# Optimization experiments

Measured on AMD Instinct MI355X. Metric: run time of the kernel, lower is better.

Reference implementation:

```python
import jax, jax.numpy as jnp
import numpy as np

N = 131072          # flattened ray-sample points
C = 32              # output_coordinate_dim per plane
BASE = 128          # base grid resolution
SCALES = [1, 2, 4]  # multiscale_res multipliers
HID = 256           # ResBlock / CondMLP hidden width
OUT = 16            # decoder output dim (geo features)
COMBS = [(0, 1), (0, 2), (1, 2)]  # itertools.combinations(range(3), 2)


def setup_inputs() -> dict:
    key = jax.random.key(0)
    ks = iter(jax.random.split(key, 64))
    inp = {}
    inp['pts'] = jax.random.uniform(next(ks), (N, 3), dtype=jnp.float32)
    inp['aabb'] = jnp.asarray([[0.0, 0.0, 0.0], [1.0, 1.0, 1.0]], dtype=jnp.float32)
    # 9 plane grids: 3 scales x 3 coordinate combinations, uniform in [0.1, 0.5)
    for s, mult in enumerate(SCALES):
        r = BASE * mult
        for ci in range(3):
            inp[f'plane_{s}_{ci}'] = jax.random.uniform(
                next(ks), (C, r, r), dtype=jnp.float32, minval=0.1, maxval=0.5)
    feat_dim = C * len(SCALES)  # concat across scales -> 96
    def lin(k, fin, fout):
        bound = 1.0 / np.sqrt(fin)
        kw, kb = jax.random.split(k)
        w = jax.random.uniform(kw, (fin, fout), dtype=jnp.float32, minval=-bound, maxval=bound)
        b = jax.random.uniform(kb, (fout,), dtype=jnp.float32, minval=-bound, maxval=bound)
        return w, b
    inp['l0_w'], inp['l0_b'] = lin(next(ks), feat_dim, HID)
    # 3 ResBlocks x 3 linears (lz, l1, l2), all 256x256 -> stacked
    rw, rb = [], []
    for _ in range(9):
        w, b = lin(next(ks), HID, HID)
        rw.append(w); rb.append(b)
    inp['res_w'] = jnp.stack(rw).reshape(3, 3, HID, HID)
    inp['res_b'] = jnp.stack(rb).reshape(3, 3, HID)
    inp['l1_w'], inp['l1_b'] = lin(next(ks), HID, OUT)
    return inp


def _bilinear(plane, xy):
    # plane: [C, H, W]; xy: [N, 2] in [-1, 1]; x -> W axis, y -> H axis
    # (F.grid_sample, align_corners=True; border clamp == zeros pad since pts in-bounds)
    Cc, H, W = plane.shape
    x = (xy[:, 0] + 1.0) * 0.5 * (W - 1)
    y = (xy[:, 1] + 1.0) * 0.5 * (H - 1)
    x0 = jnp.clip(jnp.floor(x), 0, W - 2).astype(jnp.int32)
    y0 = jnp.clip(jnp.floor(y), 0, H - 2).astype(jnp.int32)
    x1, y1 = x0 + 1, y0 + 1
    wx = (x - x0)[None, :]
    wy = (y - y0)[None, :]
    v = (plane[:, y0, x0] * (1 - wx) * (1 - wy)
         + plane[:, y0, x1] * wx * (1 - wy)
         + plane[:, y1, x0] * (1 - wx) * wy
         + plane[:, y1, x1] * wx * wy)          # [C, N]
    return v.T                                   # [N, C]


def _interp_ms(xn, planes):
    # planes: list of 3 scales, each a list of 3 [C,H,W] grids
    feats = []
    for scale_planes in planes:
        interp = 1.0
        for plane, (c0, c1) in zip(scale_planes, COMBS):
            xy = jnp.stack([xn[:, c0], xn[:, c1]], axis=-1)
            interp = interp * _bilinear(plane, xy)  # hadamard across planes
        feats.append(interp)
    return jnp.concatenate(feats, axis=-1)          # [N, C*num_scales]


def _cond_mlp(f, l0_w, l0_b, res_w, res_b, l1_w, l1_b):
    x = f @ l0_w + l0_b
    for i in range(3):
        z = jax.nn.relu(x @ res_w[i, 0] + res_b[i, 0])
        res = x + z
        x = jax.nn.relu(res @ res_w[i, 1] + res_b[i, 1])
        x = jax.nn.relu(x @ res_w[i, 2] + res_b[i, 2]) + res
    return jax.nn.sigmoid(x @ l1_w + l1_b)


def reference(pts, aabb,
              plane_0_0, plane_0_1, plane_0_2,
              plane_1_0, plane_1_1, plane_1_2,
              plane_2_0, plane_2_1, plane_2_2,
              l0_w, l0_b, res_w, res_b, l1_w, l1_b):
    xn = (pts - aabb[0]) * (2.0 / (aabb[1] - aabb[0])) - 1.0  # normalize_aabb
    planes = [[plane_0_0, plane_0_1, plane_0_2],
              [plane_1_0, plane_1_1, plane_1_2],
              [plane_2_0, plane_2_1, plane_2_2]]
    feats = _interp_ms(xn, planes)                            # [N, 96]
    return _cond_mlp(feats, l0_w, l0_b, res_w, res_b, l1_w, l1_b)  # [N, 16]
```

## Files before the change

### kernel.cpp

```cpp
#include <hip/hip_runtime.h>

typedef unsigned short u16;
typedef unsigned int u32;
typedef __attribute__((ext_vector_type(2))) unsigned int u32x2;
typedef __attribute__((ext_vector_type(8))) short short8;
typedef __attribute__((ext_vector_type(8))) _Float16 half8;
typedef __attribute__((ext_vector_type(2))) __fp16 fp16x2;
typedef __attribute__((ext_vector_type(4))) float floatx4;

__device__ __forceinline__ u16 f2h(float f){ _Float16 h = (_Float16)f; return __builtin_bit_cast(u16, h); }
__device__ __forceinline__ u32 pkrtz(float a, float b){
  fp16x2 h = __builtin_amdgcn_cvt_pkrtz(a, b);
  return __builtin_bit_cast(u32, h);
}
__device__ __forceinline__ u32 pkmax0(u32 a){
  u32 d, z = 0;
  asm("v_pk_max_f16 %0, %1, %2" : "=v"(d) : "v"(a), "v"(z));
  return d;
}
__device__ __forceinline__ u32 pkadd(u32 a, u32 b){
  u32 d;
  asm("v_pk_add_f16 %0, %1, %2" : "=v"(d) : "v"(a), "v"(b));
  return d;
}

__global__ void ptrans_kernel(const float* __restrict__ src, u16* __restrict__ dst, int HW){
  __shared__ float tile[32][257];
  const int t = threadIdx.x;
  const size_t hw0 = (size_t)blockIdx.x * 256;
  #pragma unroll
  for (int c = 0; c < 32; c++) tile[c][t] = src[(size_t)c*HW + hw0 + t];
  __syncthreads();
  u32* d32 = (u32*)(dst + hw0*32);
  #pragma unroll
  for (int i = 0; i < 16; i++){
    int idx = i*512 + t*2;
    int j = idx >> 5, cc = idx & 31;
    u32 lo = f2h(tile[cc][j]);
    u32 hi = f2h(tile[cc+1][j]);
    d32[i*256 + t] = lo | (hi << 16);
  }
}

__global__ void wconv_kernel(const float* __restrict__ src, u16* __restrict__ dst,
                             int fin, int fout, int total){
  int t = blockIdx.x*256 + threadIdx.x;
  if (t >= total) return;
  int per = fin * fout;
  int m = t / per, r = t - m*per;
  int KS = fin >> 5;
  int e = r & 7;
  int lane = (r >> 3) & 63;
  int fs = r >> 9;
  int ks = fs % KS, ft = fs / KS;
  int of = ft*16 + (lane & 15);
  int k  = ks*32 + (lane >> 4)*8 + e;
  dst[t] = f2h(src[(size_t)m*per + (size_t)k*fout + of]);
}

struct PlanePtrs { const void* p[9]; };

__global__ void interp4_kernel(const float* __restrict__ pts, const float* __restrict__ aabb,
                               PlanePtrs pp, u16* __restrict__ feats, int N)
{
  int g = blockIdx.x*256 + threadIdx.x;
  int n = g >> 2, v = g & 3;
  if (n >= N) return;
  float xn[3];
  #pragma unroll
  for (int d=0; d<3; d++){
    float lo = aabb[d], hi = aabb[3+d];
    xn[d] = (pts[(size_t)n*3 + d] - lo) * (2.0f/(hi - lo)) - 1.0f;
  }
  const int c0s[3] = {0,0,1};
  const int c1s[3] = {1,2,2};
  #pragma unroll
  for (int s=0; s<3; s++){
    const int R = 128 << s;
    float prod[8];
    #pragma unroll
    for (int p=0; p<3; p++){
      float fx = (xn[c0s[p]] + 1.0f) * 0.5f * (float)(R-1);
      float fy = (xn[c1s[p]] + 1.0f) * 0.5f * (float)(R-1);
      float fx0 = fminf(fmaxf(floorf(fx), 0.0f), (float)(R-2));
      float fy0 = fminf(fmaxf(floorf(fy), 0.0f), (float)(R-2));
      int x0 = (int)fx0, y0 = (int)fy0;
      float wx = fx - fx0, wy = fy - fy0;
      float w00 = (1.0f-wx)*(1.0f-wy), w01 = wx*(1.0f-wy);
      float w10 = (1.0f-wx)*wy,        w11 = wx*wy;
      const u16* base = (const u16*)pp.p[s*3 + p];
      const u16* b00 = base + ((size_t)y0*R + x0)*32 + v*8;
      const u16* b10 = b00 + (size_t)R*32;
      half8 h00 = *(const half8*)b00;
      half8 h01 = *(const half8*)(b00 + 32);
      half8 h10 = *(const half8*)b10;
      half8 h11 = *(const half8*)(b10 + 32);
      #pragma unroll
      for (int e=0; e<8; e++){
        float val = (float)h00[e]*w00 + (float)h01[e]*w01 + (float)h10[e]*w10 + (float)h11[e]*w11;
        prod[e] = (p == 0) ? val : prod[e]*val;
      }
    }
    short8 pk8;
    #pragma unroll
    for (int e=0; e<8; e++) pk8[e] = (short)f2h(prod[e]);
    *(short8*)(feats + (size_t)n*96 + s*32 + v*8) = pk8;
  }
}

__global__ void interp_fb_kernel(const float* __restrict__ pts, const float* __restrict__ aabb,
                                 PlanePtrs pp, u16* __restrict__ feats, int N)
{
  int n = blockIdx.x*256 + threadIdx.x;
  if (n >= N) return;
  float xn[3];
  #pragma unroll
  for (int d=0; d<3; d++){
    float lo = aabb[d], hi = aabb[3+d];
    xn[d] = (pts[(size_t)n*3 + d] - lo) * (2.0f/(hi - lo)) - 1.0f;
  }
  const int c0s[3] = {0,0,1};
  const int c1s[3] = {1,2,2};
  #pragma unroll
  for (int s=0; s<3; s++){
    const int R = 128 << s;
    float prod[32];
    #pragma unroll
    for (int p=0; p<3; p++){
      float fx = (xn[c0s[p]] + 1.0f) * 0.5f * (float)(R-1);
      float fy = (xn[c1s[p]] + 1.0f) * 0.5f * (float)(R-1);
      float fx0 = fminf(fmaxf(floorf(fx), 0.0f), (float)(R-2));
      float fy0 = fminf(fmaxf(floorf(fy), 0.0f), (float)(R-2));
      int x0 = (int)fx0, y0 = (int)fy0;
      float wx = fx - fx0, wy = fy - fy0;
      float w00 = (1.0f-wx)*(1.0f-wy), w01 = wx*(1.0f-wy);
      float w10 = (1.0f-wx)*wy,        w11 = wx*wy;
      const size_t HW = (size_t)R*R;
      const float* b00f = (const float*)pp.p[s*3+p] + (size_t)y0*R + x0;
      #pragma unroll 4
      for (int c=0; c<32; c++){
        const float* q = b00f + (size_t)c*HW;
        float val = q[0]*w00 + q[1]*w01 + q[R]*w10 + q[R+1]*w11;
        prod[c] = (p == 0) ? val : prod[c]*val;
      }
    }
    #pragma unroll
    for (int vv=0; vv<4; vv++){
      short8 pk8;
      #pragma unroll
      for (int e=0; e<8; e++) pk8[e] = (short)f2h(prod[vv*8+e]);
      *(short8*)(feats + (size_t)n*96 + s*32 + vv*8) = pk8;
    }
  }
}

template<int KSTEPS>
__device__ __forceinline__ void mm_tile(const u16* X, const u16* __restrict__ WTs,
                                        int ftbase, int lane, const floatx4 binit[4],
                                        floatx4 acc[4][4])
{
  const int lr = lane & 15, lg = lane >> 4;
  #pragma unroll
  for (int rf=0; rf<4; rf++)
    #pragma unroll
    for (int cf=0; cf<4; cf++)
      acc[rf][cf] = binit[rf];
  #pragma unroll 1
  for (int ks=0; ks<KSTEPS; ks++){
    half8 w[4];
    #pragma unroll
    for (int rf=0; rf<4; rf++)
      w[rf] = *(const half8*)(WTs + ((size_t)((ftbase+rf)*KSTEPS + ks)*64 + lane)*8);
    half8 x[4];
    #pragma unroll
    for (int cf=0; cf<4; cf++){
      int pt = cf*16 + lr;
      int byt = (pt*512 + (ks*32 + lg*8)*2) ^ ((pt & 7) << 4);
      x[cf] = *(const half8*)((const char*)X + byt);
    }
    __builtin_amdgcn_s_setprio(1);
    #pragma unroll
    for (int rf=0; rf<4; rf++)
      #pragma unroll
      for (int cf=0; cf<4; cf++)
        acc[rf][cf] = __builtin_amdgcn_mfma_f32_16x16x32_f16(w[rf], x[cf], acc[rf][cf], 0, 0, 0);
    __builtin_amdgcn_s_setprio(0);
  }
}

__device__ __forceinline__ void load_binit(const float* b, int wb, int rf16, int lg, floatx4* bi){
  #pragma unroll
  for (int rf=0; rf<4; rf++){
    float4 v = *(const float4*)(b + wb + rf*16 + lg*4);
    bi[rf] = (floatx4){v.x, v.y, v.z, v.w};
  }
  (void)rf16;
}

__global__ __launch_bounds__(256, 2) void mlp_kernel(
    const u16* __restrict__ feats,
    const u16* __restrict__ l0T, const u16* __restrict__ resT, const u16* __restrict__ l1T,
    const float* __restrict__ l0_b, const float* __restrict__ res_b, const float* __restrict__ l1_b,
    float* __restrict__ out)
{
  __shared__ u16 Xb[2][64*256];
  const int tid = threadIdx.x;
  const int wave = tid >> 6, lane = tid & 63;
  const int lr = lane & 15, lg = lane >> 4;
  const int n0 = blockIdx.x * 64;
  const int ftbase = wave * 4;
  const int wb = wave * 64;

  #pragma unroll
  for (int i=0; i<3; i++){
    int id = tid + i*256;
    int row = id / 12, sub = id - row*12;
    short8 v = *(const short8*)(feats + (size_t)(n0+row)*96 + sub*8);
    int byt = (row*512 + sub*16) ^ ((row & 7) << 4);
    *(short8*)((char*)Xb[0] + byt) = v;
  }
  __syncthreads();

  floatx4 acc[4][4];
  floatx4 binit[4];
  u32 pk[4][4][2];
  int cur = 0;

  load_binit(l0_b, wb, 0, lg, binit);
  mm_tile<3>(Xb[0], l0T, ftbase, lane, binit, acc);
  {
    char* Xw = (char*)Xb[1];
    #pragma unroll
    for (int rf=0; rf<4; rf++){
      int fby = (wb + rf*16 + lg*4)*2;
      #pragma unroll
      for (int cf=0; cf<4; cf++){
        int pt = cf*16 + lr;
        u32 p0 = pkrtz(acc[rf][cf][0], acc[rf][cf][1]);
        u32 p1 = pkrtz(acc[rf][cf][2], acc[rf][cf][3]);
        pk[rf][cf][0] = p0; pk[rf][cf][1] = p1;
        int byt = (pt*512 + fby) ^ ((pt & 7) << 4);
        *(u32x2*)(Xw + byt) = (u32x2){p0, p1};
      }
    }
  }
  __syncthreads();
  cur = 1;

  for (int rb=0; rb<3; rb++){
    const u16* W0 = resT + (size_t)(rb*3+0)*65536;
    const u16* W1 = resT + (size_t)(rb*3+1)*65536;
    const u16* W2 = resT + (size_t)(rb*3+2)*65536;
    const float* b0 = res_b + (rb*3+0)*256;
    const float* b1 = res_b + (rb*3+1)*256;
    const float* b2 = res_b + (rb*3+2)*256;

    load_binit(b0, wb, 0, lg, binit);
    mm_tile<8>(Xb[cur], W0, ftbase, lane, binit, acc);
    {
      char* Xw = (char*)Xb[cur^1];
      #pragma unroll
      for (int rf=0; rf<4; rf++){
        int fby = (wb + rf*16 + lg*4)*2;
        #pragma unroll
        for (int cf=0; cf<4; cf++){
          int pt = cf*16 + lr;
          u32 p0 = pkadd(pk[rf][cf][0], pkmax0(pkrtz(acc[rf][cf][0], acc[rf][cf][1])));
          u32 p1 = pkadd(pk[rf][cf][1], pkmax0(pkrtz(acc[rf][cf][2], acc[rf][cf][3])));
          pk[rf][cf][0] = p0; pk[rf][cf][1] = p1;
          int byt = (pt*512 + fby) ^ ((pt & 7) << 4);
          *(u32x2*)(Xw + byt) = (u32x2){p0, p1};
        }
      }
    }
    __syncthreads();
    cur ^= 1;

    load_binit(b1, wb, 0, lg, binit);
    mm_tile<8>(Xb[cur], W1, ftbase, lane, binit, acc);
    {
      char* Xw = (char*)Xb[cur^1];
      #pragma unroll
      for (int rf=0; rf<4; rf++){
        int fby = (wb + rf*16 + lg*4)*2;
        #pragma unroll
        for (int cf=0; cf<4; cf++){
          int pt = cf*16 + lr;
          u32 p0 = pkmax0(pkrtz(acc[rf][cf][0], acc[rf][cf][1]));
          u32 p1 = pkmax0(pkrtz(acc[rf][cf][2], acc[rf][cf][3]));
          int byt = (pt*512 + fby) ^ ((pt & 7) << 4);
          *(u32x2*)(Xw + byt) = (u32x2){p0, p1};
        }
      }
    }
    __syncthreads();
    cur ^= 1;

    load_binit(b2, wb, 0, lg, binit);
    mm_tile<8>(Xb[cur], W2, ftbase, lane, binit, acc);
    {
      char* Xw = (char*)Xb[cur^1];
      #pragma unroll
      for (int rf=0; rf<4; rf++){
        int fby = (wb + rf*16 + lg*4)*2;
        #pragma unroll
        for (int cf=0; cf<4; cf++){
          int pt = cf*16 + lr;
          u32 p0 = pkadd(pkmax0(pkrtz(acc[rf][cf][0], acc[rf][cf][1])), pk[rf][cf][0]);
          u32 p1 = pkadd(pkmax0(pkrtz(acc[rf][cf][2], acc[rf][cf][3])), pk[rf][cf][1]);
          pk[rf][cf][0] = p0; pk[rf][cf][1] = p1;
          int byt = (pt*512 + fby) ^ ((pt & 7) << 4);
          *(u32x2*)(Xw + byt) = (u32x2){p0, p1};
        }
      }
    }
    __syncthreads();
    cur ^= 1;
  }

  floatx4 accf;
  {
    float4 bo = *(const float4*)(l1_b + lg*4);
    accf = (floatx4){bo.x, bo.y, bo.z, bo.w};
  }
  const char* Xr = (const char*)Xb[cur];
  #pragma unroll 1
  for (int ks=0; ks<8; ks++){
    int pt = wave*16 + lr;
    int byt = (pt*512 + (ks*32 + lg*8)*2) ^ ((pt&7)<<4);
    half8 x = *(const half8*)(Xr + byt);
    half8 w = *(const half8*)(l1T + ((size_t)ks*64 + lane)*8);
    accf = __builtin_amdgcn_mfma_f32_16x16x32_f16(w, x, accf, 0, 0, 0);
  }
  {
    float4 o;
    o.x = 1.0f / (1.0f + __expf(-accf[0]));
    o.y = 1.0f / (1.0f + __expf(-accf[1]));
    o.z = 1.0f / (1.0f + __expf(-accf[2]));
    o.w = 1.0f / (1.0f + __expf(-accf[3]));
    *(float4*)(out + (size_t)(n0 + wave*16 + lr)*16 + lg*4) = o;
  }
}

extern "C" void kernel_launch(void* const* d_in, const int* in_sizes, int n_in,
                              void* d_out, int out_size, void* d_ws, size_t ws_size,
                              hipStream_t stream)
{
  const float* pts  = (const float*)d_in[0];
  const float* aabb = (const float*)d_in[1];
  const float* l0_w = (const float*)d_in[11];
  const float* res_w= (const float*)d_in[13];
  const float* l1_w = (const float*)d_in[15];
  const float* l0_b = (const float*)d_in[12];
  const float* res_b= (const float*)d_in[14];
  const float* l1_b = (const float*)d_in[16];
  const int N = in_sizes[0] / 3;

  char* ws = (char*)d_ws;
  const size_t woff_l0  = 0;
  const size_t woff_res = 49152;
  const size_t woff_l1  = woff_res + 9*65536*2;
  const size_t foff     = woff_l1 + 8192;
  const size_t poff     = foff + (size_t)N*96*2;

  static const int HWs[3] = {128*128, 256*256, 512*512};
  size_t pel[9]; size_t tot = 0;
  for (int s=0;s<3;s++) for (int p=0;p<3;p++){ pel[s*3+p] = tot; tot += (size_t)HWs[s]*32; }

  const bool tr_mode = (ws_size >= poff + tot*2);

  wconv_kernel<<<(24576+255)/256,  256, 0, stream>>>(l0_w, (u16*)(ws+woff_l0), 96, 256, 24576);
  wconv_kernel<<<(589824+255)/256, 256, 0, stream>>>(res_w,(u16*)(ws+woff_res),256, 256, 589824);
  wconv_kernel<<<(4096+255)/256,   256, 0, stream>>>(l1_w, (u16*)(ws+woff_l1), 256, 16,  4096);

  PlanePtrs pp;
  if (tr_mode){
    u16* pbase = (u16*)(ws + poff);
    for (int i=0;i<9;i++){
      int s = i/3;
      ptrans_kernel<<<HWs[s]/256, 256, 0, stream>>>((const float*)d_in[2+i], pbase + pel[i], HWs[s]);
      pp.p[i] = pbase + pel[i];
    }
    interp4_kernel<<<(4*N+255)/256, 256, 0, stream>>>(pts, aabb, pp, (u16*)(ws+foff), N);
  } else {
    for (int i=0;i<9;i++) pp.p[i] = d_in[2+i];
    interp_fb_kernel<<<(N+255)/256, 256, 0, stream>>>(pts, aabb, pp, (u16*)(ws+foff), N);
  }

  mlp_kernel<<<N/64, 256, 0, stream>>>((const u16*)(ws+foff),
      (const u16*)(ws+woff_l0), (const u16*)(ws+woff_res), (const u16*)(ws+woff_l1),
      l0_b, res_b, l1_b, (float*)d_out);
}
```

Before: 270.9 us.

## Fuse plane interpolation into MLP kernel and batch conversion launches

Moves the bilinear multi-plane gather into the MLP kernel's prologue, so features are written straight to shared memory instead of round-tripping through a global feats buffer. It also merges the nine plane-transpose launches into one kernel and the three weight-conversion launches into one, which cuts launch overhead. The cost is extra gather latency inside an occupancy-limited MLP kernel (launch bounds 256,2), which has no separate interp kernel to hide that latency behind.

After: 252.3 us. 6.9% less time.

```diff
diff --git a/kernel.cpp b/kernel.cpp
--- a/kernel.cpp
+++ b/kernel.cpp
@@ -24,28 +24,35 @@
   return d;
 }
 
-__global__ void ptrans_kernel(const float* __restrict__ src, u16* __restrict__ dst, int HW){
+struct PlanePtrs { const void* p[9]; };
+struct PtransArgs { const float* src[9]; u16* dst[9]; int blk0[10]; int HW[9]; };
+
+__global__ void ptrans_all_kernel(PtransArgs a){
   __shared__ float tile[32][257];
+  int bi = blockIdx.x;
+  int i = 0;
+  #pragma unroll
+  for (int k = 1; k < 9; k++) if (bi >= a.blk0[k]) i = k;
+  const float* src = a.src[i];
+  u16* dst = a.dst[i];
+  const int HW = a.HW[i];
   const int t = threadIdx.x;
-  const size_t hw0 = (size_t)blockIdx.x * 256;
+  const size_t hw0 = (size_t)(bi - a.blk0[i]) * 256;
   #pragma unroll
   for (int c = 0; c < 32; c++) tile[c][t] = src[(size_t)c*HW + hw0 + t];
   __syncthreads();
   u32* d32 = (u32*)(dst + hw0*32);
   #pragma unroll
-  for (int i = 0; i < 16; i++){
-    int idx = i*512 + t*2;
+  for (int k = 0; k < 16; k++){
+    int idx = k*512 + t*2;
     int j = idx >> 5, cc = idx & 31;
     u32 lo = f2h(tile[cc][j]);
     u32 hi = f2h(tile[cc+1][j]);
-    d32[i*256 + t] = lo | (hi << 16);
-  }
-}
-
-__global__ void wconv_kernel(const float* __restrict__ src, u16* __restrict__ dst,
-                             int fin, int fout, int total){
-  int t = blockIdx.x*256 + threadIdx.x;
-  if (t >= total) return;
+    d32[k*256 + t] = lo | (hi << 16);
+  }
+}
+
+__device__ __forceinline__ void wconv_one(const float* src, u16* dst, int fin, int fout, int t){
   int per = fin * fout;
   int m = t / per, r = t - m*per;
   int KS = fin >> 5;
@@ -57,55 +64,14 @@
   int k  = ks*32 + (lane >> 4)*8 + e;
   dst[t] = f2h(src[(size_t)m*per + (size_t)k*fout + of]);
 }
-
-struct PlanePtrs { const void* p[9]; };
-
-__global__ void interp4_kernel(const float* __restrict__ pts, const float* __restrict__ aabb,
-                               PlanePtrs pp, u16* __restrict__ feats, int N)
-{
-  int g = blockIdx.x*256 + threadIdx.x;
-  int n = g >> 2, v = g & 3;
-  if (n >= N) return;
-  float xn[3];
-  #pragma unroll
-  for (int d=0; d<3; d++){
-    float lo = aabb[d], hi = aabb[3+d];
-    xn[d] = (pts[(size_t)n*3 + d] - lo) * (2.0f/(hi - lo)) - 1.0f;
-  }
-  const int c0s[3] = {0,0,1};
-  const int c1s[3] = {1,2,2};
-  #pragma unroll
-  for (int s=0; s<3; s++){
-    const int R = 128 << s;
-    float prod[8];
-    #pragma unroll
-    for (int p=0; p<3; p++){
-      float fx = (xn[c0s[p]] + 1.0f) * 0.5f * (float)(R-1);
-      float fy = (xn[c1s[p]] + 1.0f) * 0.5f * (float)(R-1);
-      float fx0 = fminf(fmaxf(floorf(fx), 0.0f), (float)(R-2));
-      float fy0 = fminf(fmaxf(floorf(fy), 0.0f), (float)(R-2));
-      int x0 = (int)fx0, y0 = (int)fy0;
-      float wx = fx - fx0, wy = fy - fy0;
-      float w00 = (1.0f-wx)*(1.0f-wy), w01 = wx*(1.0f-wy);
-      float w10 = (1.0f-wx)*wy,        w11 = wx*wy;
-      const u16* base = (const u16*)pp.p[s*3 + p];
-      const u16* b00 = base + ((size_t)y0*R + x0)*32 + v*8;
-      const u16* b10 = b00 + (size_t)R*32;
-      half8 h00 = *(const half8*)b00;
-      half8 h01 = *(const half8*)(b00 + 32);
-      half8 h10 = *(const half8*)b10;
-      half8 h11 = *(const half8*)(b10 + 32);
-      #pragma unroll
-      for (int e=0; e<8; e++){
-        float val = (float)h00[e]*w00 + (float)h01[e]*w01 + (float)h10[e]*w10 + (float)h11[e]*w11;
-        prod[e] = (p == 0) ? val : prod[e]*val;
-      }
-    }
-    short8 pk8;
-    #pragma unroll
-    for (int e=0; e<8; e++) pk8[e] = (short)f2h(prod[e]);
-    *(short8*)(feats + (size_t)n*96 + s*32 + v*8) = pk8;
-  }
+__global__ void wconv_all_kernel(const float* l0_w, const float* res_w, const float* l1_w,
+                                 u16* l0T, u16* resT, u16* l1T){
+  int t = blockIdx.x*256 + threadIdx.x;
+  if (t < 24576){ wconv_one(l0_w, l0T, 96, 256, t); return; }
+  t -= 24576;
+  if (t < 589824){ wconv_one(res_w, resT, 256, 256, t); return; }
+  t -= 589824;
+  if (t < 4096){ wconv_one(l1_w, l1T, 256, 16, t); }
 }
 
 __global__ void interp_fb_kernel(const float* __restrict__ pts, const float* __restrict__ aabb,
@@ -188,16 +154,17 @@
   }
 }
 
-__device__ __forceinline__ void load_binit(const float* b, int wb, int rf16, int lg, floatx4* bi){
+__device__ __forceinline__ void load_binit(const float* b, int wb, int lg, floatx4* bi){
   #pragma unroll
   for (int rf=0; rf<4; rf++){
     float4 v = *(const float4*)(b + wb + rf*16 + lg*4);
     bi[rf] = (floatx4){v.x, v.y, v.z, v.w};
   }
-  (void)rf16;
-}
-
+}
+
+template<bool GATHER>
 __global__ __launch_bounds__(256, 2) void mlp_kernel(
+    const float* __restrict__ pts, const float* __restrict__ aabb, PlanePtrs pp,
     const u16* __restrict__ feats,
     const u16* __restrict__ l0T, const u16* __restrict__ resT, const u16* __restrict__ l1T,
     const float* __restrict__ l0_b, const float* __restrict__ res_b, const float* __restrict__ l1_b,
@@ -211,13 +178,59 @@
   const int ftbase = wave * 4;
   const int wb = wave * 64;
 
-  #pragma unroll
-  for (int i=0; i<3; i++){
-    int id = tid + i*256;
-    int row = id / 12, sub = id - row*12;
-    short8 v = *(const short8*)(feats + (size_t)(n0+row)*96 + sub*8);
-    int byt = (row*512 + sub*16) ^ ((row & 7) << 4);
-    *(short8*)((char*)Xb[0] + byt) = v;
+  if constexpr (GATHER){
+    const int pt = tid >> 2, v = tid & 3;
+    const int n = n0 + pt;
+    float xn[3];
+    #pragma unroll
+    for (int d=0; d<3; d++){
+      float lo = aabb[d], hi = aabb[3+d];
+      xn[d] = (pts[(size_t)n*3 + d] - lo) * (2.0f/(hi - lo)) - 1.0f;
+    }
+    const int c0s[3] = {0,0,1};
+    const int c1s[3] = {1,2,2};
+    #pragma unroll
+    for (int s=0; s<3; s++){
+      const int R = 128 << s;
+      float prod[8];
+      #pragma unroll
+      for (int p=0; p<3; p++){
+        float fx = (xn[c0s[p]] + 1.0f) * 0.5f * (float)(R-1);
+        float fy = (xn[c1s[p]] + 1.0f) * 0.5f * (float)(R-1);
+        float fx0 = fminf(fmaxf(floorf(fx), 0.0f), (float)(R-2));
+        float fy0 = fminf(fmaxf(floorf(fy), 0.0f), (float)(R-2));
+        int x0 = (int)fx0, y0 = (int)fy0;
+        float wx = fx - fx0, wy = fy - fy0;
+        float w00 = (1.0f-wx)*(1.0f-wy), w01 = wx*(1.0f-wy);
+        float w10 = (1.0f-wx)*wy,        w11 = wx*wy;
+        const u16* base = (const u16*)pp.p[s*3 + p];
+        const u16* b00 = base + ((size_t)y0*R + x0)*32 + v*8;
+        const u16* b10 = b00 + (size_t)R*32;
+        half8 h00 = *(const half8*)b00;
+        half8 h01 = *(const half8*)(b00 + 32);
+        half8 h10 = *(const half8*)b10;
+        half8 h11 = *(const half8*)(b10 + 32);
+        #pragma unroll
+        for (int e=0; e<8; e++){
+          float val = (float)h00[e]*w00 + (float)h01[e]*w01 + (float)h10[e]*w10 + (float)h11[e]*w11;
+          prod[e] = (p == 0) ? val : prod[e]*val;
+        }
+      }
+      short8 pk8;
+      #pragma unroll
+      for (int e=0; e<8; e++) pk8[e] = (short)f2h(prod[e]);
+      int byt = (pt*512 + (s*32 + v*8)*2) ^ ((pt & 7) << 4);
+      *(short8*)((char*)Xb[0] + byt) = pk8;
+    }
+  } else {
+    #pragma unroll
+    for (int i=0; i<3; i++){
+      int id = tid + i*256;
+      int row = id / 12, sub = id - row*12;
+      short8 v = *(const short8*)(feats + (size_t)(n0+row)*96 + sub*8);
+      int byt = (row*512 + sub*16) ^ ((row & 7) << 4);
+      *(short8*)((char*)Xb[0] + byt) = v;
+    }
   }
   __syncthreads();
 
@@ -226,7 +239,7 @@
   u32 pk[4][4][2];
   int cur = 0;
 
-  load_binit(l0_b, wb, 0, lg, binit);
+  load_binit(l0_b, wb, lg, binit);
   mm_tile<3>(Xb[0], l0T, ftbase, lane, binit, acc);
   {
     char* Xw = (char*)Xb[1];
@@ -255,7 +268,7 @@
     const float* b1 = res_b + (rb*3+1)*256;
     const float* b2 = res_b + (rb*3+2)*256;
 
-    load_binit(b0, wb, 0, lg, binit);
+    load_binit(b0, wb, lg, binit);
     mm_tile<8>(Xb[cur], W0, ftbase, lane, binit, acc);
     {
       char* Xw = (char*)Xb[cur^1];
@@ -276,7 +289,7 @@
     __syncthreads();
     cur ^= 1;
 
-    load_binit(b1, wb, 0, lg, binit);
+    load_binit(b1, wb, lg, binit);
     mm_tile<8>(Xb[cur], W1, ftbase, lane, binit, acc);
     {
       char* Xw = (char*)Xb[cur^1];
@@ -296,7 +309,7 @@
     __syncthreads();
     cur ^= 1;
 
-    load_binit(b2, wb, 0, lg, binit);
+    load_binit(b2, wb, lg, binit);
     mm_tile<8>(Xb[cur], W2, ftbase, lane, binit, acc);
     {
       char* Xw = (char*)Xb[cur^1];
@@ -369,25 +382,33 @@
 
   const bool tr_mode = (ws_size >= poff + tot*2);
 
-  wconv_kernel<<<(24576+255)/256,  256, 0, stream>>>(l0_w, (u16*)(ws+woff_l0), 96, 256, 24576);
-  wconv_kernel<<<(589824+255)/256, 256, 0, stream>>>(res_w,(u16*)(ws+woff_res),256, 256, 589824);
-  wconv_kernel<<<(4096+255)/256,   256, 0, stream>>>(l1_w, (u16*)(ws+woff_l1), 256, 16,  4096);
+  wconv_all_kernel<<<(24576+589824+4096+255)/256, 256, 0, stream>>>(
+      l0_w, res_w, l1_w, (u16*)(ws+woff_l0), (u16*)(ws+woff_res), (u16*)(ws+woff_l1));
 
   PlanePtrs pp;
   if (tr_mode){
     u16* pbase = (u16*)(ws + poff);
+    PtransArgs pa;
+    int b0 = 0;
     for (int i=0;i<9;i++){
       int s = i/3;
-      ptrans_kernel<<<HWs[s]/256, 256, 0, stream>>>((const float*)d_in[2+i], pbase + pel[i], HWs[s]);
+      pa.src[i] = (const float*)d_in[2+i];
+      pa.dst[i] = pbase + pel[i];
+      pa.blk0[i] = b0;
+      pa.HW[i] = HWs[s];
+      b0 += HWs[s]/256;
       pp.p[i] = pbase + pel[i];
     }
-    interp4_kernel<<<(4*N+255)/256, 256, 0, stream>>>(pts, aabb, pp, (u16*)(ws+foff), N);
+    pa.blk0[9] = b0;
+    ptrans_all_kernel<<<b0, 256, 0, stream>>>(pa);
+    mlp_kernel<true><<<N/64, 256, 0, stream>>>(pts, aabb, pp, (const u16*)nullptr,
+        (const u16*)(ws+woff_l0), (const u16*)(ws+woff_res), (const u16*)(ws+woff_l1),
+        l0_b, res_b, l1_b, (float*)d_out);
   } else {
     for (int i=0;i<9;i++) pp.p[i] = d_in[2+i];
     interp_fb_kernel<<<(N+255)/256, 256, 0, stream>>>(pts, aabb, pp, (u16*)(ws+foff), N);
-  }
-
-  mlp_kernel<<<N/64, 256, 0, stream>>>((const u16*)(ws+foff),
-      (const u16*)(ws+woff_l0), (const u16*)(ws+woff_res), (const u16*)(ws+woff_l1),
-      l0_b, res_b, l1_b, (float*)d_out);
-}
+    mlp_kernel<false><<<N/64, 256, 0, stream>>>(pts, aabb, pp, (const u16*)(ws+foff),
+        (const u16*)(ws+woff_l0), (const u16*)(ws+woff_res), (const u16*)(ws+woff_l1),
+        l0_b, res_b, l1_b, (float*)d_out);
+  }
+}
```
